# Kernel optimization log

Hardware: AMD Instinct MI355X
Metric: run time of the kernel (lower is better)

The kernel has to match this reference:

```python
import jax, jax.numpy as jnp
import numpy as np

N_BATCH, T = 65536, 256
SURROGATE_SLOPE = 5.0


def setup_inputs() -> dict:
    key = jax.random.key(0)
    k1, k2, k3, k4 = jax.random.split(key, 4)
    x = jax.random.normal(k1, (N_BATCH, T), dtype=jnp.float32)
    beta = jax.random.normal(k2, (), dtype=jnp.float32)
    threshold = jax.random.uniform(k3, (), dtype=jnp.float32)  # kept positive like a sane threshold init
    init_rand = jax.random.uniform(k4, (N_BATCH,), dtype=jnp.float32)  # torch.rand(N_batch)
    return {"x": x, "beta": beta, "threshold": threshold, "init_rand": init_rand}


def reference(x, beta, threshold, init_rand):
    # feasible_beta = sigmoid(beta); forward uses RAW threshold (not softplus)
    fb = jax.nn.sigmoid(beta)
    # memory init: rand * threshold.detach()
    m0 = init_rand * jax.lax.stop_gradient(threshold)

    def step(m, xt):
        m_new = fb * m + xt                      # StateUpdate
        surplus = m_new - threshold
        hard = (surplus >= 0).astype(x.dtype)    # forward spike
        soft = jax.nn.sigmoid(surplus * SURROGATE_SLOPE)  # surrogate grad path
        spike = jax.lax.stop_gradient(hard) + soft - jax.lax.stop_gradient(soft)
        m_post = m_new - jax.lax.stop_gradient(spike) * threshold  # StatePostupdate
        # torch records the PRE-step memory (initial m0, then previous post-update m)
        return m_post, (spike, m)

    _, (spikes_tn, mems_tn) = jax.lax.scan(step, m0, x.T)  # scan over T
    return spikes_tn.T, mems_tn.T  # each (N_batch, T)
```

## Files before the change

### kernel.cpp

```cpp
#include <hip/hip_runtime.h>
#include <math.h>


#define N_BATCH 65536
#define T_STEPS 256
#define ROWS    64
#define CHUNK   64
#define NCHUNK  (T_STEPS / CHUNK)
#define C4      (CHUNK / 4)
#define STRIDE  (CHUNK + 1)

#define LDS_FENCE() asm volatile("s_waitcnt lgkmcnt(0)" ::: "memory")

typedef float f32x4 __attribute__((ext_vector_type(4)));

__global__ __launch_bounds__(64) void snn_fwd_kernel(
    const float* __restrict__ x,
    const float* __restrict__ beta_p,
    const float* __restrict__ thr_p,
    const float* __restrict__ init_rand,
    float* __restrict__ out)
{
#pragma clang fp contract(off)
    __shared__ float ss[ROWS * STRIDE];
    __shared__ float ms[ROWS * STRIDE];

    const int t   = threadIdx.x;
    const int row = blockIdx.x * ROWS + t;

    const float thr = thr_p[0];
    const float fb = (float)(1.0 / (1.0 + exp(-(double)beta_p[0])));

    float m = init_rand[row] * thr;

    const f32x4* __restrict__ xr =
        reinterpret_cast<const f32x4*>(x) + (size_t)row * (T_STEPS / 4);
    float* __restrict__ s_out = out;
    float* __restrict__ m_out = out + (size_t)N_BATCH * T_STEPS;

    f32x4 xbuf[C4];
#pragma unroll
    for (int i = 0; i < C4; ++i) xbuf[i] = xr[i];

#pragma unroll
    for (int cc = 0; cc < NCHUNK; ++cc) {
        f32x4 xnext[C4];
        if (cc + 1 < NCHUNK) {
#pragma unroll
            for (int i = 0; i < C4; ++i) xnext[i] = xr[(cc + 1) * C4 + i];
        }

        float* __restrict__ srow = ss + t * STRIDE;
        float* __restrict__ mrow = ms + t * STRIDE;
#pragma unroll
        for (int i = 0; i < C4; ++i) {
            const f32x4 xv = xbuf[i];
#pragma unroll
            for (int j = 0; j < 4; ++j) {
                mrow[4 * i + j] = m;
                float prod = fb * m;
                float mn   = prod + xv[j];
                float su   = mn - thr;
                srow[4 * i + j] = (su >= 0.0f) ? 1.0f : 0.0f;
                m = (su >= 0.0f) ? su : mn;
            }
        }
        LDS_FENCE();

        const int k = t & 15;
#pragma unroll
        for (int p = 0; p < 16; ++p) {
            const int rr = (t >> 4) + 4 * p;
            const int la = rr * STRIDE + 4 * k;
            f32x4 sv, mv;
            sv.x = ss[la];     sv.y = ss[la + 1];
            sv.z = ss[la + 2]; sv.w = ss[la + 3];
            mv.x = ms[la];     mv.y = ms[la + 1];
            mv.z = ms[la + 2]; mv.w = ms[la + 3];
            const size_t g = (size_t)(blockIdx.x * ROWS + rr) * T_STEPS
                           + cc * CHUNK + 4 * k;
            __builtin_nontemporal_store(sv, reinterpret_cast<f32x4*>(s_out + g));
            __builtin_nontemporal_store(mv, reinterpret_cast<f32x4*>(m_out + g));
        }
        LDS_FENCE();

        if (cc + 1 < NCHUNK) {
#pragma unroll
            for (int i = 0; i < C4; ++i) xbuf[i] = xnext[i];
        }
    }
}

extern "C" void kernel_launch(void* const* d_in, const int* in_sizes, int n_in,
                              void* d_out, int out_size, void* d_ws, size_t ws_size,
                              hipStream_t stream) {
    const float* x         = (const float*)d_in[0];
    const float* beta      = (const float*)d_in[1];
    const float* threshold = (const float*)d_in[2];
    const float* init_rand = (const float*)d_in[3];
    float* out             = (float*)d_out;

    const int threads = ROWS;
    const int blocks  = N_BATCH / ROWS;
    snn_fwd_kernel<<<blocks, threads, 0, stream>>>(x, beta, threshold, init_rand, out);
}
```

Measured before the change: 36.18 us.

## Coalesce x loads through an LDS transpose and halve the chunk size

Each thread used to load its own row of x with strided per-thread vector loads. Now the wavefront loads x cooperatively and coalesced: 8 threads cover each row segment, the tile is staged into a padded LDS tile, and each thread then reads its row back from LDS for the sequential scan. The chunk size drops from 64 to 32 to cut register and LDS use for the prefetch buffers. This adds LDS traffic, extra fences and more chunk iterations.

New measurement: 34.89 us. 1.04x faster.

```diff
diff --git a/kernel.cpp b/kernel.cpp
--- a/kernel.cpp
+++ b/kernel.cpp
@@ -5,10 +5,10 @@
 #define N_BATCH 65536
 #define T_STEPS 256
 #define ROWS    64
-#define CHUNK   64
+#define CHUNK   32
 #define NCHUNK  (T_STEPS / CHUNK)
-#define C4      (CHUNK / 4)
 #define STRIDE  (CHUNK + 1)
+#define XPL     8
 
 #define LDS_FENCE() asm volatile("s_waitcnt lgkmcnt(0)" ::: "memory")
 
@@ -22,6 +22,7 @@
     float* __restrict__ out)
 {
 #pragma clang fp contract(off)
+    __shared__ float xs[ROWS * STRIDE];
     __shared__ float ss[ROWS * STRIDE];
     __shared__ float ms[ROWS * STRIDE];
 
@@ -33,44 +34,61 @@
 
     float m = init_rand[row] * thr;
 
-    const f32x4* __restrict__ xr =
-        reinterpret_cast<const f32x4*>(x) + (size_t)row * (T_STEPS / 4);
     float* __restrict__ s_out = out;
     float* __restrict__ m_out = out + (size_t)N_BATCH * T_STEPS;
 
-    f32x4 xbuf[C4];
+    const int k  = t & 7;
+    const int r0 = t >> 3;
+
+    {
+        f32x4 xld[XPL];
 #pragma unroll
-    for (int i = 0; i < C4; ++i) xbuf[i] = xr[i];
+        for (int q = 0; q < XPL; ++q) {
+            const int rr = r0 + 8 * q;
+            xld[q] = *reinterpret_cast<const f32x4*>(
+                x + (size_t)(blockIdx.x * ROWS + rr) * T_STEPS + 4 * k);
+        }
+#pragma unroll
+        for (int q = 0; q < XPL; ++q) {
+            const int rr = r0 + 8 * q;
+            const int la = rr * STRIDE + 4 * k;
+            xs[la]     = xld[q].x; xs[la + 1] = xld[q].y;
+            xs[la + 2] = xld[q].z; xs[la + 3] = xld[q].w;
+        }
+        LDS_FENCE();
+    }
 
 #pragma unroll
     for (int cc = 0; cc < NCHUNK; ++cc) {
-        f32x4 xnext[C4];
+        f32x4 xnext[XPL];
         if (cc + 1 < NCHUNK) {
 #pragma unroll
-            for (int i = 0; i < C4; ++i) xnext[i] = xr[(cc + 1) * C4 + i];
+            for (int q = 0; q < XPL; ++q) {
+                const int rr = r0 + 8 * q;
+                xnext[q] = *reinterpret_cast<const f32x4*>(
+                    x + (size_t)(blockIdx.x * ROWS + rr) * T_STEPS
+                      + (cc + 1) * CHUNK + 4 * k);
+            }
         }
 
+        float* __restrict__ xrow = xs + t * STRIDE;
         float* __restrict__ srow = ss + t * STRIDE;
         float* __restrict__ mrow = ms + t * STRIDE;
 #pragma unroll
-        for (int i = 0; i < C4; ++i) {
-            const f32x4 xv = xbuf[i];
-#pragma unroll
-            for (int j = 0; j < 4; ++j) {
-                mrow[4 * i + j] = m;
-                float prod = fb * m;
-                float mn   = prod + xv[j];
-                float su   = mn - thr;
-                srow[4 * i + j] = (su >= 0.0f) ? 1.0f : 0.0f;
-                m = (su >= 0.0f) ? su : mn;
-            }
+        for (int i = 0; i < CHUNK; ++i) {
+            const float xv = xrow[i];
+            mrow[i] = m;
+            float prod = fb * m;
+            float mn   = prod + xv;
+            float su   = mn - thr;
+            srow[i] = (su >= 0.0f) ? 1.0f : 0.0f;
+            m = (su >= 0.0f) ? su : mn;
         }
         LDS_FENCE();
 
-        const int k = t & 15;
 #pragma unroll
-        for (int p = 0; p < 16; ++p) {
-            const int rr = (t >> 4) + 4 * p;
+        for (int p = 0; p < 8; ++p) {
+            const int rr = r0 + 8 * p;
             const int la = rr * STRIDE + 4 * k;
             f32x4 sv, mv;
             sv.x = ss[la];     sv.y = ss[la + 1];
@@ -86,7 +104,13 @@
 
         if (cc + 1 < NCHUNK) {
 #pragma unroll
-            for (int i = 0; i < C4; ++i) xbuf[i] = xnext[i];
+            for (int q = 0; q < XPL; ++q) {
+                const int rr = r0 + 8 * q;
+                const int la = rr * STRIDE + 4 * k;
+                xs[la]     = xnext[q].x; xs[la + 1] = xnext[q].y;
+                xs[la + 2] = xnext[q].z; xs[la + 3] = xnext[q].w;
+            }
+            LDS_FENCE();
         }
     }
 }
```
